# Kernel tuning notes

Hardware: AMD Instinct MI355X
Metric: run time of the kernel (lower is better)

The kernel has to match this reference:

```python
import jax, jax.numpy as jnp
import numpy as np

EMBED_DIM = 768
NUM_HEADS = 12
HEAD_DIM = EMBED_DIM // NUM_HEADS


def setup_inputs() -> dict:
    key = jax.random.key(0)
    ks = jax.random.split(key, 5)
    B, N, D = 8, 1024, EMBED_DIM
    s = 1.0 / np.sqrt(D)
    x = jax.random.normal(ks[0], (B, N, D), dtype=jnp.float32)
    W_qkv = jax.random.normal(ks[1], (D, 3 * D), dtype=jnp.float32) * s
    b_qkv = jnp.zeros((3 * D,), dtype=jnp.float32)
    W_proj = jax.random.normal(ks[2], (D, D), dtype=jnp.float32) * s
    b_proj = jnp.zeros((D,), dtype=jnp.float32)
    return {"x": x, "W_qkv": W_qkv, "b_qkv": b_qkv, "W_proj": W_proj, "b_proj": b_proj}


def reference(x, W_qkv, b_qkv, W_proj, b_proj):
    B, N, D = x.shape
    H, Hd = NUM_HEADS, HEAD_DIM
    scale = Hd ** -0.5
    qkv = x @ W_qkv + b_qkv                      # (B, N, 3D)
    qkv = qkv.reshape(B, N, 3, H, Hd).transpose(2, 0, 3, 1, 4)  # (3, B, H, N, Hd)
    q, k, v = qkv[0], qkv[1], qkv[2]
    attn = jnp.einsum('bhnd,bhmd->bhnm', q, k) * scale  # (B, H, N, N)
    attn = jax.nn.softmax(attn, axis=-1)
    out = jnp.einsum('bhnm,bhmd->bhnd', attn, v)        # (B, H, N, Hd)
    out = out.transpose(0, 2, 1, 3).reshape(B, N, D)
    return out @ W_proj + b_proj
```

## Files before the change

kernel.cpp:

```cpp
#include <hip/hip_runtime.h>


#define B_   8
#define N_   1024
#define D_   768
#define H_   12
#define HD_  64

typedef __attribute__((ext_vector_type(4))) float f32x4;
typedef __attribute__((ext_vector_type(16))) float f32x16;
typedef __attribute__((ext_vector_type(8))) short bf16x8;
typedef __attribute__((ext_vector_type(2))) unsigned int u32x2;
typedef __attribute__((ext_vector_type(4))) unsigned int u32x4;

__device__ __forceinline__ unsigned short f2bf(float f) {
    unsigned int u = __float_as_uint(f);
    u += 0x7fff + ((u >> 16) & 1);
    return (unsigned short)(u >> 16);
}
__device__ __forceinline__ unsigned int pk2(float a, float b) {
    return (unsigned int)f2bf(a) | ((unsigned int)f2bf(b) << 16);
}
__device__ __forceinline__ unsigned int pk2t(float a, float b) {
    return __builtin_amdgcn_perm(__float_as_uint(b), __float_as_uint(a), 0x07060302u);
}
__device__ __forceinline__ float truncbf(float f) {
    return __uint_as_float(__float_as_uint(f) & 0xFFFF0000u);
}
__device__ __forceinline__ void gl_lds16(const void* g, void* l) {
    __builtin_amdgcn_global_load_lds(
        (const __attribute__((address_space(1))) unsigned int*)g,
        (__attribute__((address_space(3))) unsigned int*)l, 16, 0, 0);
}
#define MFMA(a, b, c)   __builtin_amdgcn_mfma_f32_16x16x32_bf16(a, b, c, 0, 0, 0)
#define MFMA32(a, b, c) __builtin_amdgcn_mfma_f32_32x32x16_bf16(a, b, c, 0, 0, 0)
#define BAR() do { __asm__ volatile("" ::: "memory"); \
    __builtin_amdgcn_s_barrier(); \
    __asm__ volatile("" ::: "memory"); } while (0)
#define WAITVM(n) do { __asm__ volatile("" ::: "memory"); \
    __builtin_amdgcn_s_waitcnt(0xF70 | (n)); \
    __asm__ volatile("" ::: "memory"); } while (0)

__global__ __launch_bounds__(256) void prep_kernel(
    const float* __restrict__ x, const float* __restrict__ wqkv,
    const float* __restrict__ wproj,
    unsigned short* __restrict__ XB, unsigned short* __restrict__ WQT,
    unsigned short* __restrict__ WPT)
{
    const int bid = blockIdx.x;
    const int tid = threadIdx.x;
    if (bid < 3072) {
        int id = bid * 256 + tid;
        int r  = id & 127;
        int kc = (id >> 7) & 7;
        int ks = (id >> 10) % 12;
        int nt = id / 12288;
        const float* src = x + (size_t)(nt * 128 + r) * 768 + ks * 64 + kc * 8;
        float4 f0 = *(const float4*)src;
        float4 f1 = *(const float4*)(src + 4);
        uint4 o;
        o.x = pk2(f0.x, f0.y); o.y = pk2(f0.z, f0.w);
        o.z = pk2(f1.x, f1.y); o.w = pk2(f1.z, f1.w);
        *(uint4*)&XB[(size_t)id * 8] = o;
    } else if (bid < 3936) {
        int id = (bid - 3072) * 256 + tid;
        int fr = id & 127;
        int kc = (id >> 7) & 7;
        int ks = (id >> 10) % 12;
        int mt = id / 12288;
        float v[8];
#pragma unroll
        for (int j = 0; j < 8; ++j)
            v[j] = wqkv[(size_t)(ks * 64 + kc * 8 + j) * 2304 + mt * 128 + fr];
        uint4 o;
        o.x = pk2(v[0], v[1]); o.y = pk2(v[2], v[3]);
        o.z = pk2(v[4], v[5]); o.w = pk2(v[6], v[7]);
        *(uint4*)&WQT[(size_t)id * 8] = o;
    } else {
        int id = (bid - 3936) * 256 + tid;
        int fr = id & 63;
        int kc = (id >> 6) & 7;
        int ks = (id >> 9) % 12;
        int nt = id / 6144;
        float v[8];
#pragma unroll
        for (int j = 0; j < 8; ++j)
            v[j] = wproj[(size_t)(ks * 64 + kc * 8 + j) * 768 + nt * 64 + fr];
        uint4 o;
        o.x = pk2(v[0], v[1]); o.y = pk2(v[2], v[3]);
        o.z = pk2(v[4], v[5]); o.w = pk2(v[6], v[7]);
        *(uint4*)&WPT[(size_t)id * 8] = o;
    }
}

__global__ __launch_bounds__(256, 4) void qkv_gemm(
    const unsigned short* __restrict__ XB,
    const unsigned short* __restrict__ WQT,
    const float* __restrict__ bias,
    unsigned short* __restrict__ QS,
    unsigned short* __restrict__ KS,
    unsigned short* __restrict__ VS)
{
    __shared__ __align__(16) unsigned short sm[16384];

    const int tid = threadIdx.x;
    const int w = tid >> 6, lane = tid & 63;
    const int l15 = lane & 15, quad = lane >> 4;
    const int mt = blockIdx.x >> 6;
    const int nt = blockIdx.x & 63;
    const int m0w = (w & 1) * 64, n0w = (w >> 1) * 64;
    const float CS = 0.18033688f;

    char* smb = (char*)sm;
    const char* baseA = (const char*)(WQT + (size_t)(mt * 12) * 8192);
    const char* baseB = (const char*)(XB  + (size_t)(nt * 12) * 8192);

    auto issue = [&](int ks) {
        const char* sA = baseA + ks * 8192;
        const char* sB = baseB + ks * 8192;
        const int pb = ks & 1;
#pragma unroll
        for (int i = 0; i < 2; ++i) {
            const int c = w * 2 + i;
            gl_lds16(sA + (c * 64 + lane) * 16, smb + pb * 8192 + c * 1024);
            gl_lds16(sB + (c * 64 + lane) * 16, smb + 16384 + pb * 8192 + c * 1024);
        }
    };

    f32x4 acc[4][4];
    const f32x4 z = {0.f, 0.f, 0.f, 0.f};
#pragma unroll
    for (int t = 0; t < 4; ++t)
#pragma unroll
        for (int u = 0; u < 4; ++u) acc[t][u] = z;

    issue(0);
    WAITVM(0);
    BAR();
    for (int ks = 0; ks < 24; ++ks) {
        if (ks < 23) issue(ks + 1);
        const unsigned short* Ab = sm + (ks & 1) * 4096;
        const unsigned short* Bb = sm + 8192 + (ks & 1) * 4096;
        bf16x8 af[4], bfv[4];
#pragma unroll
        for (int t = 0; t < 4; ++t)
            af[t] = *(const bf16x8*)(Ab + (quad * 128 + m0w + t * 16 + l15) * 8);
#pragma unroll
        for (int u = 0; u < 4; ++u)
            bfv[u] = *(const bf16x8*)(Bb + (quad * 128 + n0w + u * 16 + l15) * 8);
#pragma unroll
        for (int t = 0; t < 4; ++t)
#pragma unroll
            for (int u = 0; u < 4; ++u)
                acc[t][u] = MFMA(af[t], bfv[u], acc[t][u]);
        if (ks < 23) { WAITVM(0); BAR(); }
    }

    const int part = mt / 6;
    BAR();

#pragma unroll
    for (int t = 0; t < 4; ++t) {
        int d = m0w + t * 16 + quad * 4;
        float4 bv = *(const float4*)&bias[part * 768 + (mt % 6) * 128 + d];
#pragma unroll
        for (int u = 0; u < 4; ++u) {
            int tok = n0w + u * 16 + l15;
            f32x4 a = acc[t][u];
            float v0 = a[0] + bv.x, v1 = a[1] + bv.y;
            float v2 = a[2] + bv.z, v3 = a[3] + bv.w;
            if (part == 0) { v0 *= CS; v1 *= CS; v2 *= CS; v3 *= CS; }
            if (part < 2) {
                unsigned off = tok * 256 + (((unsigned)(d * 2)) ^ ((tok & 7) << 4));
                uint2 pp; pp.x = pk2(v0, v1); pp.y = pk2(v2, v3);
                *(uint2*)(smb + off) = pp;
            } else {
                float vv[4] = {v0, v1, v2, v3};
#pragma unroll
                for (int r4 = 0; r4 < 4; ++r4) {
                    int dd = d + r4;
                    unsigned off = dd * 256 + (((unsigned)(tok * 2)) ^ ((dd & 7) << 4));
                    *(unsigned short*)(smb + off) = f2bf(vv[r4]);
                }
            }
        }
    }
    BAR();

    const int b = nt >> 3, qtc = nt & 7;
    if (part == 0) {
#pragma unroll
        for (int round = 0; round < 8; ++round) {
            int r = tid & 127;
            int kc = (tid >> 7) + round * 2;
            uint4 val = *(const uint4*)(smb + r * 256 +
                        (((unsigned)(kc << 4)) ^ ((r & 7) << 4)));
            int h = (mt % 6) * 2 + (kc >> 3);
            int bh = b * H_ + h;
            *(uint4*)(QS + (((size_t)(bh * 8 + qtc) * 1024) + (kc & 7) * 128 + r) * 8) = val;
        }
    } else if (part == 1) {
#pragma unroll
        for (int round = 0; round < 8; ++round) {
            int r = tid & 127;
            int kc = (tid >> 7) + round * 2;
            uint4 val = *(const uint4*)(smb + r * 256 +
                        (((unsigned)(kc << 4)) ^ ((r & 7) << 4)));
            int h = (mt % 6) * 2 + (kc >> 3);
            int bh = b * H_ + h;
            int kt = (qtc << 1) | (r >> 6);
            *(uint4*)(KS + (((size_t)(bh * 16 + kt) * 512) + (kc & 7) * 64 + (r & 63)) * 8) = val;
        }
    } else {
#pragma unroll
        for (int round = 0; round < 8; ++round) {
            int dd = tid & 127;
            int tc = (tid >> 7) + round * 2;
            uint4 val = *(const uint4*)(smb + dd * 256 +
                        (((unsigned)(tc << 4)) ^ ((dd & 7) << 4)));
            int h = (mt % 6) * 2 + (dd >> 6);
            int bh = b * H_ + h;
            int kt = (qtc << 1) | (tc >> 3);
            *(uint4*)(VS + (((size_t)(bh * 16 + kt) * 512) + (tc & 7) * 64 + (dd & 63)) * 8) = val;
        }
    }
}

__global__ __launch_bounds__(256, 3) void attn_kernel(
    const unsigned short* __restrict__ QS,
    const unsigned short* __restrict__ KS,
    const unsigned short* __restrict__ VS,
    unsigned short* __restrict__ AWS)
{
    __shared__ __align__(16) unsigned short sm[24576];
    const int tid = threadIdx.x;
    const int w = tid >> 6, lane = tid & 63;
    const int l31 = lane & 31, h = lane >> 5;
    const int bh = blockIdx.x % 96;
    const int qt = blockIdx.x / 96;

    char* smb = (char*)sm;
    const char* kbase = (const char*)(KS + (size_t)(bh * 16) * 4096);
    const char* vbase = (const char*)(VS + (size_t)(bh * 16) * 4096);

    auto issue_tile = [&](int kt) {
        const char* ks_ = kbase + kt * 8192;
        const char* vs_ = vbase + kt * 8192;
        const int sl = kt % 3;
#pragma unroll
        for (int i = 0; i < 2; ++i) {
            const int c = w * 2 + i;
            gl_lds16(ks_ + (c * 64 + lane) * 16, smb + sl * 8192 + c * 1024);
            gl_lds16(vs_ + (c * 64 + lane) * 16, smb + 24576 + sl * 8192 + c * 1024);
        }
    };

    const char* qslab = (const char*)(QS + (size_t)(bh * 8 + qt) * 8192);
    bf16x8 qf[4];
#pragma unroll
    for (int ks = 0; ks < 4; ++ks)
        qf[ks] = *(const bf16x8*)(qslab +
                 (((ks * 2 + h) * 128) + w * 32 + l31) * 16);

    issue_tile(0);
    issue_tile(1);
    WAITVM(4);
    BAR();

    f32x16 acc[2];
    const f32x16 z16 = {0.f,0.f,0.f,0.f,0.f,0.f,0.f,0.f,
                        0.f,0.f,0.f,0.f,0.f,0.f,0.f,0.f};
    acc[0] = z16; acc[1] = z16;
    float lsum = 0.f;

    for (int kt = 0; kt < 16; ++kt) {
        if (kt < 14) issue_tile(kt + 2);

        const char* Kb = smb + (kt % 3) * 8192;
        const char* Vb = smb + 24576 + (kt % 3) * 8192;

        f32x16 sv[2] = {z16, z16};
        __builtin_amdgcn_s_setprio(1);
#pragma unroll
        for (int ks = 0; ks < 4; ++ks) {
#pragma unroll
            for (int kb = 0; kb < 2; ++kb) {
                bf16x8 kf = *(const bf16x8*)(Kb +
                            ((ks * 2 + h) * 64 + kb * 32 + l31) * 16);
                sv[kb] = MFMA32(kf, qf[ks], sv[kb]);
            }
        }
        __builtin_amdgcn_s_setprio(0);

        unsigned pw[4][4];
#pragma unroll
        for (int kb = 0; kb < 2; ++kb) {
            float p[16];
#pragma unroll
            for (int r = 0; r < 16; ++r)
                p[r] = truncbf(__builtin_amdgcn_exp2f(sv[kb][r]));
            lsum += ((((p[0] + p[1]) + (p[2] + p[3])) +
                      ((p[4] + p[5]) + (p[6] + p[7]))) +
                     (((p[8] + p[9]) + (p[10] + p[11])) +
                      ((p[12] + p[13]) + (p[14] + p[15]))));
            unsigned X0 = pk2t(p[0],  p[1]),  X1 = pk2t(p[2],  p[3]);
            unsigned Y0 = pk2t(p[4],  p[5]),  Y1 = pk2t(p[6],  p[7]);
            unsigned Z0 = pk2t(p[8],  p[9]),  Z1 = pk2t(p[10], p[11]);
            unsigned W0 = pk2t(p[12], p[13]), W1 = pk2t(p[14], p[15]);
            u32x2 a0 = __builtin_amdgcn_permlane32_swap(X0, Y0, false, false);
            u32x2 a1 = __builtin_amdgcn_permlane32_swap(X1, Y1, false, false);
            u32x2 b0 = __builtin_amdgcn_permlane32_swap(Z0, W0, false, false);
            u32x2 b1 = __builtin_amdgcn_permlane32_swap(Z1, W1, false, false);
            pw[kb * 2][0] = a0[0]; pw[kb * 2][1] = a1[0];
            pw[kb * 2][2] = a0[1]; pw[kb * 2][3] = a1[1];
            pw[kb * 2 + 1][0] = b0[0]; pw[kb * 2 + 1][1] = b1[0];
            pw[kb * 2 + 1][2] = b0[1]; pw[kb * 2 + 1][3] = b1[1];
        }

        __builtin_amdgcn_s_setprio(1);
#pragma unroll
        for (int ks = 0; ks < 4; ++ks) {
            u32x4 pv = {pw[ks][0], pw[ks][1], pw[ks][2], pw[ks][3]};
            bf16x8 pf = __builtin_bit_cast(bf16x8, pv);
#pragma unroll
            for (int db = 0; db < 2; ++db) {
                bf16x8 vf = *(const bf16x8*)(Vb +
                            ((ks * 2 + h) * 64 + db * 32 + l31) * 16);
                acc[db] = MFMA32(vf, pf, acc[db]);
            }
        }
        __builtin_amdgcn_s_setprio(0);

        if (kt < 14)       { WAITVM(4); BAR(); }
        else if (kt == 14) { WAITVM(0); BAR(); }
    }

    float lfull = lsum + __shfl_xor(lsum, 32, 64);
    float inv = 1.f / lfull;

    const int b = bh / H_, hh = bh % H_;
    const int mtA = b * 8 + qt;
    unsigned short* obase = AWS + (size_t)(mtA * 12 + hh) * 8192;
#pragma unroll
    for (int db = 0; db < 2; ++db) {
#pragma unroll
        for (int gp = 0; gp < 2; ++gp) {
            const int g0 = gp * 2, g1 = gp * 2 + 1;
            unsigned v00 = pk2(acc[db][4 * g0 + 0] * inv, acc[db][4 * g0 + 1] * inv);
            unsigned v01 = pk2(acc[db][4 * g0 + 2] * inv, acc[db][4 * g0 + 3] * inv);
            unsigned v10 = pk2(acc[db][4 * g1 + 0] * inv, acc[db][4 * g1 + 1] * inv);
            unsigned v11 = pk2(acc[db][4 * g1 + 2] * inv, acc[db][4 * g1 + 3] * inv);
            u32x2 t0 = __builtin_amdgcn_permlane32_swap(v00, v10, false, false);
            u32x2 t1 = __builtin_amdgcn_permlane32_swap(v01, v11, false, false);
            uint4 val;
            val.x = t0[0]; val.y = t1[0]; val.z = t0[1]; val.w = t1[1];
            const int dc = db * 4 + g0 + h;
            *(uint4*)(obase + ((size_t)(dc * 128) + w * 32 + l31) * 8) = val;
        }
    }
}

__global__ __launch_bounds__(256, 3) void proj_gemm(
    const unsigned short* __restrict__ AWS,
    const unsigned short* __restrict__ WPT,
    const float* __restrict__ bias, float* __restrict__ out)
{
    __shared__ __align__(16) unsigned short As[2][8192];
    __shared__ __align__(16) unsigned short Bs[2][4096];

    const int tid = threadIdx.x;
    const int w = tid >> 6, lane = tid & 63;
    const int l15 = lane & 15, quad = lane >> 4;
    const int mt = blockIdx.x / 12;
    const int nt = blockIdx.x % 12;
    const int m0w = (w & 1) * 64, n0w = (w >> 1) * 32;

    const char* baseA = (const char*)(AWS + (size_t)(mt * 12) * 8192);
    const char* baseB = (const char*)(WPT + (size_t)(nt * 12) * 4096);

    auto issue = [&](int ks) {
        const char* sA = baseA + ks * 16384;
        const char* sB = baseB + ks * 8192;
        const int pb = ks & 1;
#pragma unroll
        for (int i = 0; i < 4; ++i) {
            const int c = w * 4 + i;
            gl_lds16(sA + (c * 64 + lane) * 16, (char*)As + pb * 16384 + c * 1024);
        }
#pragma unroll
        for (int i = 0; i < 2; ++i) {
            const int c = w * 2 + i;
            gl_lds16(sB + (c * 64 + lane) * 16, (char*)Bs + pb * 8192 + c * 1024);
        }
    };

    f32x4 acc[4][2];
    const f32x4 z = {0.f, 0.f, 0.f, 0.f};
#pragma unroll
    for (int t = 0; t < 4; ++t) { acc[t][0] = z; acc[t][1] = z; }

    issue(0);
    WAITVM(0);
    BAR();
    for (int ks = 0; ks < 12; ++ks) {
        if (ks < 11) issue(ks + 1);
        const unsigned short* Ab = As[ks & 1];
        const unsigned short* Bb = Bs[ks & 1];
#pragma unroll
        for (int kk = 0; kk < 2; ++kk) {
            bf16x8 af[4], bfv[2];
#pragma unroll
            for (int t = 0; t < 4; ++t)
                af[t] = *(const bf16x8*)(Ab + (((kk * 4 + quad) * 128) + m0w + t * 16 + l15) * 8);
#pragma unroll
            for (int u = 0; u < 2; ++u)
                bfv[u] = *(const bf16x8*)(Bb + (((kk * 4 + quad) * 64) + n0w + u * 16 + l15) * 8);
#pragma unroll
            for (int t = 0; t < 4; ++t)
#pragma unroll
                for (int u = 0; u < 2; ++u)
                    acc[t][u] = MFMA(af[t], bfv[u], acc[t][u]);
        }
        if (ks < 11) { WAITVM(0); BAR(); }
    }

#pragma unroll
    for (int t = 0; t < 4; ++t)
#pragma unroll
        for (int u = 0; u < 2; ++u) {
            int col = nt * 64 + n0w + u * 16 + l15;
            float bvv = bias[col];
#pragma unroll
            for (int r = 0; r < 4; ++r) {
                int row = mt * 128 + m0w + t * 16 + quad * 4 + r;
                out[(size_t)row * 768 + col] = acc[t][u][r] + bvv;
            }
        }
}

extern "C" void kernel_launch(void* const* d_in, const int* in_sizes, int n_in,
                              void* d_out, int out_size, void* d_ws, size_t ws_size,
                              hipStream_t stream) {
    const float* x     = (const float*)d_in[0];
    const float* Wqkv  = (const float*)d_in[1];
    const float* bqkv  = (const float*)d_in[2];
    const float* Wproj = (const float*)d_in[3];
    const float* bproj = (const float*)d_in[4];
    float* out = (float*)d_out;

    unsigned short* ws = (unsigned short*)d_ws;
    unsigned short* XB  = ws;
    unsigned short* WQT = ws + 6291456;
    unsigned short* WPT = ws + 8060928;
    unsigned short* QS  = ws + 8650752;
    unsigned short* KS  = ws + 14942208;
    unsigned short* VS  = ws + 21233664;
    unsigned short* AWS = ws + 27525120;

    prep_kernel<<<dim3(4224), dim3(256), 0, stream>>>(x, Wqkv, Wproj, XB, WQT, WPT);
    qkv_gemm<<<dim3(18 * 64), dim3(256), 0, stream>>>(XB, WQT, bqkv, QS, KS, VS);
    attn_kernel<<<dim3(96 * 8), dim3(256), 0, stream>>>(QS, KS, VS, AWS);
    proj_gemm<<<dim3(64 * 12), dim3(256), 0, stream>>>(AWS, WPT, bproj, out);
}
```

Measured before the change: 182.1 us.

## Software-pipeline attention QK with softmax/PV and restructure GEMM load waits

Attention loop is unrolled by two so the QK^T MFMAs for the next key tile are issued before softmax and PV of the current tile, letting exp/pack work overlap with matrix ops. The QKV and projection GEMM loops now wait only for the previous stage's loads (partial vmcnt) between two barriers instead of fully draining after each issue. This adds extra barriers per GEMM iteration and more live registers in attention, and the three-slot ring with tile kt+3 issued after a full drain must stay hazard-free.

```diff
diff --git a/kernel.cpp b/kernel.cpp
--- a/kernel.cpp
+++ b/kernel.cpp
@@ -135,10 +135,10 @@
         for (int u = 0; u < 4; ++u) acc[t][u] = z;
 
     issue(0);
-    WAITVM(0);
-    BAR();
     for (int ks = 0; ks < 24; ++ks) {
-        if (ks < 23) issue(ks + 1);
+        BAR();
+        if (ks < 23) { issue(ks + 1); WAITVM(4); } else { WAITVM(0); }
+        BAR();
         const unsigned short* Ab = sm + (ks & 1) * 4096;
         const unsigned short* Bb = sm + 8192 + (ks & 1) * 4096;
         bf16x8 af[4], bfv[4];
@@ -153,7 +153,6 @@
 #pragma unroll
             for (int u = 0; u < 4; ++u)
                 acc[t][u] = MFMA(af[t], bfv[u], acc[t][u]);
-        if (ks < 23) { WAITVM(0); BAR(); }
     }
 
     const int part = mt / 6;
@@ -264,7 +263,7 @@
 
     issue_tile(0);
     issue_tile(1);
-    WAITVM(4);
+    WAITVM(0);
     BAR();
 
     f32x16 acc[2];
@@ -273,67 +272,94 @@
     acc[0] = z16; acc[1] = z16;
     float lsum = 0.f;
 
-    for (int kt = 0; kt < 16; ++kt) {
+#define QK_CLUSTER(SV, TILE)                                               \
+    do {                                                                   \
+        const char* Kb_ = smb + ((TILE) % 3) * 8192;                       \
+        __builtin_amdgcn_s_setprio(1);                                     \
+        _Pragma("unroll")                                                  \
+        for (int ks = 0; ks < 4; ++ks) {                                   \
+            _Pragma("unroll")                                              \
+            for (int kb = 0; kb < 2; ++kb) {                               \
+                bf16x8 kf = *(const bf16x8*)(Kb_ +                         \
+                            ((ks * 2 + h) * 64 + kb * 32 + l31) * 16);     \
+                SV[kb] = MFMA32(kf, qf[ks], SV[kb]);                       \
+            }                                                              \
+        }                                                                  \
+        __builtin_amdgcn_s_setprio(0);                                     \
+    } while (0)
+
+#define SM_CLUSTER(SV, PW)                                                 \
+    do {                                                                   \
+        _Pragma("unroll")                                                  \
+        for (int kb = 0; kb < 2; ++kb) {                                   \
+            float p[16];                                                   \
+            _Pragma("unroll")                                              \
+            for (int r = 0; r < 16; ++r)                                   \
+                p[r] = truncbf(__builtin_amdgcn_exp2f(SV[kb][r]));         \
+            lsum += ((((p[0] + p[1]) + (p[2] + p[3])) +                    \
+                      ((p[4] + p[5]) + (p[6] + p[7]))) +                   \
+                     (((p[8] + p[9]) + (p[10] + p[11])) +                  \
+                      ((p[12] + p[13]) + (p[14] + p[15]))));               \
+            unsigned X0 = pk2t(p[0],  p[1]),  X1 = pk2t(p[2],  p[3]);      \
+            unsigned Y0 = pk2t(p[4],  p[5]),  Y1 = pk2t(p[6],  p[7]);      \
+            unsigned Z0 = pk2t(p[8],  p[9]),  Z1 = pk2t(p[10], p[11]);     \
+            unsigned W0 = pk2t(p[12], p[13]), W1 = pk2t(p[14], p[15]);     \
+            u32x2 a0 = __builtin_amdgcn_permlane32_swap(X0, Y0, false, false); \
+            u32x2 a1 = __builtin_amdgcn_permlane32_swap(X1, Y1, false, false); \
+            u32x2 b0 = __builtin_amdgcn_permlane32_swap(Z0, W0, false, false); \
+            u32x2 b1 = __builtin_amdgcn_permlane32_swap(Z1, W1, false, false); \
+            PW[kb * 2][0] = a0[0]; PW[kb * 2][1] = a1[0];                  \
+            PW[kb * 2][2] = a0[1]; PW[kb * 2][3] = a1[1];                  \
+            PW[kb * 2 + 1][0] = b0[0]; PW[kb * 2 + 1][1] = b1[0];          \
+            PW[kb * 2 + 1][2] = b0[1]; PW[kb * 2 + 1][3] = b1[1];          \
+        }                                                                  \
+    } while (0)
+
+#define PV_CLUSTER(PW, TILE)                                               \
+    do {                                                                   \
+        const char* Vb_ = smb + 24576 + ((TILE) % 3) * 8192;               \
+        __builtin_amdgcn_s_setprio(1);                                     \
+        _Pragma("unroll")                                                  \
+        for (int ks = 0; ks < 4; ++ks) {                                   \
+            u32x4 pv = {PW[ks][0], PW[ks][1], PW[ks][2], PW[ks][3]};       \
+            bf16x8 pf = __builtin_bit_cast(bf16x8, pv);                    \
+            _Pragma("unroll")                                              \
+            for (int db = 0; db < 2; ++db) {                               \
+                bf16x8 vf = *(const bf16x8*)(Vb_ +                         \
+                            ((ks * 2 + h) * 64 + db * 32 + l31) * 16);     \
+                acc[db] = MFMA32(vf, pf, acc[db]);                         \
+            }                                                              \
+        }                                                                  \
+        __builtin_amdgcn_s_setprio(0);                                     \
+    } while (0)
+
+    f32x16 svA[2] = {z16, z16};
+    f32x16 svB[2] = {z16, z16};
+    QK_CLUSTER(svA, 0);
+
+    for (int kt = 0; kt < 16; kt += 2) {
         if (kt < 14) issue_tile(kt + 2);
-
-        const char* Kb = smb + (kt % 3) * 8192;
-        const char* Vb = smb + 24576 + (kt % 3) * 8192;
-
-        f32x16 sv[2] = {z16, z16};
-        __builtin_amdgcn_s_setprio(1);
-#pragma unroll
-        for (int ks = 0; ks < 4; ++ks) {
-#pragma unroll
-            for (int kb = 0; kb < 2; ++kb) {
-                bf16x8 kf = *(const bf16x8*)(Kb +
-                            ((ks * 2 + h) * 64 + kb * 32 + l31) * 16);
-                sv[kb] = MFMA32(kf, qf[ks], sv[kb]);
-            }
-        }
-        __builtin_amdgcn_s_setprio(0);
-
-        unsigned pw[4][4];
-#pragma unroll
-        for (int kb = 0; kb < 2; ++kb) {
-            float p[16];
-#pragma unroll
-            for (int r = 0; r < 16; ++r)
-                p[r] = truncbf(__builtin_amdgcn_exp2f(sv[kb][r]));
-            lsum += ((((p[0] + p[1]) + (p[2] + p[3])) +
-                      ((p[4] + p[5]) + (p[6] + p[7]))) +
-                     (((p[8] + p[9]) + (p[10] + p[11])) +
-                      ((p[12] + p[13]) + (p[14] + p[15]))));
-            unsigned X0 = pk2t(p[0],  p[1]),  X1 = pk2t(p[2],  p[3]);
-            unsigned Y0 = pk2t(p[4],  p[5]),  Y1 = pk2t(p[6],  p[7]);
-            unsigned Z0 = pk2t(p[8],  p[9]),  Z1 = pk2t(p[10], p[11]);
-            unsigned W0 = pk2t(p[12], p[13]), W1 = pk2t(p[14], p[15]);
-            u32x2 a0 = __builtin_amdgcn_permlane32_swap(X0, Y0, false, false);
-            u32x2 a1 = __builtin_amdgcn_permlane32_swap(X1, Y1, false, false);
-            u32x2 b0 = __builtin_amdgcn_permlane32_swap(Z0, W0, false, false);
-            u32x2 b1 = __builtin_amdgcn_permlane32_swap(Z1, W1, false, false);
-            pw[kb * 2][0] = a0[0]; pw[kb * 2][1] = a1[0];
-            pw[kb * 2][2] = a0[1]; pw[kb * 2][3] = a1[1];
-            pw[kb * 2 + 1][0] = b0[0]; pw[kb * 2 + 1][1] = b1[0];
-            pw[kb * 2 + 1][2] = b0[1]; pw[kb * 2 + 1][3] = b1[1];
-        }
-
-        __builtin_amdgcn_s_setprio(1);
-#pragma unroll
-        for (int ks = 0; ks < 4; ++ks) {
-            u32x4 pv = {pw[ks][0], pw[ks][1], pw[ks][2], pw[ks][3]};
-            bf16x8 pf = __builtin_bit_cast(bf16x8, pv);
-#pragma unroll
-            for (int db = 0; db < 2; ++db) {
-                bf16x8 vf = *(const bf16x8*)(Vb +
-                            ((ks * 2 + h) * 64 + db * 32 + l31) * 16);
-                acc[db] = MFMA32(vf, pf, acc[db]);
-            }
-        }
-        __builtin_amdgcn_s_setprio(0);
-
-        if (kt < 14)       { WAITVM(4); BAR(); }
-        else if (kt == 14) { WAITVM(0); BAR(); }
-    }
+        svB[0] = z16; svB[1] = z16;
+        QK_CLUSTER(svB, kt + 1);
+        unsigned pwA[4][4];
+        SM_CLUSTER(svA, pwA);
+        PV_CLUSTER(pwA, kt);
+        if (kt < 14) { WAITVM(0); BAR(); }
+
+        if (kt < 14) {
+            issue_tile(kt + 3);
+            svA[0] = z16; svA[1] = z16;
+            QK_CLUSTER(svA, kt + 2);
+        }
+        unsigned pwB[4][4];
+        SM_CLUSTER(svB, pwB);
+        PV_CLUSTER(pwB, kt + 1);
+        if (kt < 14) { WAITVM(0); BAR(); }
+    }
+
+#undef QK_CLUSTER
+#undef SM_CLUSTER
+#undef PV_CLUSTER
 
     float lfull = lsum + __shfl_xor(lsum, 32, 64);
     float inv = 1.f / lfull;
@@ -400,10 +426,10 @@
     for (int t = 0; t < 4; ++t) { acc[t][0] = z; acc[t][1] = z; }
 
     issue(0);
-    WAITVM(0);
-    BAR();
     for (int ks = 0; ks < 12; ++ks) {
-        if (ks < 11) issue(ks + 1);
+        BAR();
+        if (ks < 11) { issue(ks + 1); WAITVM(6); } else { WAITVM(0); }
+        BAR();
         const unsigned short* Ab = As[ks & 1];
         const unsigned short* Bb = Bs[ks & 1];
 #pragma unroll
@@ -421,7 +447,6 @@
                 for (int u = 0; u < 2; ++u)
                     acc[t][u] = MFMA(af[t], bfv[u], acc[t][u]);
         }
-        if (ks < 11) { WAITVM(0); BAR(); }
     }
 
 #pragma unroll
```

New measurement: 198.6 us. 1.09x slower.
